# Performance work log

Measured on AMD Instinct MI355X. Metric: run time of the kernel, lower is better.

## Reference

```python
import jax, jax.numpy as jnp
import numpy as np

N1, N2, C = 1024, 1024, 128
H = 2 * C  # h_dim = in_dim * 2


def setup_inputs() -> dict:
    key = jax.random.key(0)
    ks = jax.random.split(key, 8)
    std = 0.01
    return {
        "X": jax.random.normal(ks[0], (N1, C), dtype=jnp.float32),
        "Y": jax.random.normal(ks[1], (N2, C), dtype=jnp.float32),
        "Wsr": jax.random.normal(ks[2], (C, C), dtype=jnp.float32) * std,
        "Wtg": jax.random.normal(ks[3], (C, C), dtype=jnp.float32) * std,
        "W1": jax.random.normal(ks[4], (H, H), dtype=jnp.float32) * std,
        "b1": jnp.zeros((H,), dtype=jnp.float32),
        "W2": jax.random.normal(ks[5], (1, H), dtype=jnp.float32) * std,
        "b2": jnp.zeros((1,), dtype=jnp.float32),
    }


def reference(X, Y, Wsr, Wtg, W1, b1, W2, b2):
    # project_sr / project_tg (bias-free Linear: x @ W^T)
    Xp = X @ Wsr.T  # [N1, C]
    Yp = Y @ Wtg.T  # [N2, C]
    # First fc_M linear on concat([X_k, Y_k]) == split-weight form:
    # concat(x, y) @ W1^T = x @ W1[:, :C]^T + y @ W1[:, C:]^T
    Xh = Xp @ W1[:, :C].T  # [N1, 2C]
    Yh = Yp @ W1[:, C:].T  # [N2, 2C]
    Hid = jax.nn.relu(Xh[:, None, :] + Yh[None, :, :] + b1)  # [N1, N2, 2C]
    # Second linear 2C -> 1, then squeeze
    M = jnp.einsum('abh,h->ab', Hid, W2[0]) + b2[0]  # [N1, N2]
    return M
```

## Files before the change

### kernel.cpp

```cpp
#include <hip/hip_runtime.h>

#define N1 1024
#define N2 1024
#define CDIM 128
#define HDIM 256


__global__ __launch_bounds__(256) void fold_weights(
    const float* __restrict__ W1, const float* __restrict__ Wsr,
    const float* __restrict__ Wtg, float* __restrict__ Wx,
    float* __restrict__ Wy) {
  int id = blockIdx.x * 256 + threadIdx.x;
  int m  = id / (HDIM * CDIM);
  int r  = id % (HDIM * CDIM);
  int h  = r / CDIM;
  int j  = r % CDIM;
  const float* Wm    = m ? Wtg : Wsr;
  const float* w1row = W1 + (size_t)h * HDIM + (m ? CDIM : 0);
  float acc = 0.f;
#pragma unroll 8
  for (int c = 0; c < CDIM; ++c)
    acc = fmaf(w1row[c], Wm[(size_t)c * CDIM + j], acc);
  (m ? Wy : Wx)[(size_t)h * CDIM + j] = acc;
}

__global__ __launch_bounds__(256) void gemm_ht(
    const float* __restrict__ X, const float* __restrict__ Y,
    const float* __restrict__ Wx, const float* __restrict__ Wy,
    const float* __restrict__ b1, float* __restrict__ XhT,
    float* __restrict__ YhT) {
  const float* A = blockIdx.z ? Y : X;
  const float* W = blockIdx.z ? Wy : Wx;
  float*       O = blockIdx.z ? YhT : XhT;
  const bool useBias = (blockIdx.z == 0);

  __shared__ float Al[64][132];
  __shared__ float Wl[128][68];

  const int t  = threadIdx.x;
  const int n0 = blockIdx.x * 64;
  const int h0 = blockIdx.y * 64;

#pragma unroll
  for (int it = 0; it < 8; ++it) {
    int row = it * 8 + (t >> 5);
    int col = (t & 31) * 4;
    *(float4*)(&Al[row][col]) =
        *(const float4*)(&A[(size_t)(n0 + row) * CDIM + col]);
  }
#pragma unroll
  for (int it = 0; it < 8; ++it) {
    int h = it * 8 + (t >> 5);
    int k = (t & 31) * 4;
    float4 w = *(const float4*)(&W[(size_t)(h0 + h) * CDIM + k]);
    Wl[k + 0][h] = w.x;
    Wl[k + 1][h] = w.y;
    Wl[k + 2][h] = w.z;
    Wl[k + 3][h] = w.w;
  }
  __syncthreads();

  const int tx = t & 15;
  const int ty = t >> 4;
  float acc[4][4];
#pragma unroll
  for (int i = 0; i < 4; ++i)
#pragma unroll
    for (int j = 0; j < 4; ++j) acc[i][j] = 0.f;

  for (int k4 = 0; k4 < CDIM; k4 += 4) {
    float a_[4][4];
#pragma unroll
    for (int i = 0; i < 4; ++i) {
      float4 v = *(const float4*)(&Al[ty * 4 + i][k4]);
      a_[i][0] = v.x; a_[i][1] = v.y; a_[i][2] = v.z; a_[i][3] = v.w;
    }
#pragma unroll
    for (int kk = 0; kk < 4; ++kk) {
      float4 w = *(const float4*)(&Wl[k4 + kk][tx * 4]);
      float wj[4] = {w.x, w.y, w.z, w.w};
#pragma unroll
      for (int i = 0; i < 4; ++i)
#pragma unroll
        for (int j = 0; j < 4; ++j)
          acc[i][j] = fmaf(a_[i][kk], wj[j], acc[i][j]);
    }
  }

#pragma unroll
  for (int j = 0; j < 4; ++j) {
    int h = h0 + tx * 4 + j;
    float b = useBias ? b1[h] : 0.f;
    float4 v = {acc[0][j] + b, acc[1][j] + b, acc[2][j] + b, acc[3][j] + b};
    *(float4*)(&O[(size_t)h * N1 + n0 + ty * 4]) = v;
  }
}

__global__ __launch_bounds__(256, 4) void pairwise_half(
    const float* __restrict__ XhT, const float* __restrict__ YhT,
    const float* __restrict__ W2, float* __restrict__ Pbase) {
  __shared__ float Xl[64][64];
  __shared__ float Yl[64][64];

  const int t  = threadIdx.x;
  const int b0 = blockIdx.x * 64;
  const int a0 = blockIdx.y * 64;
  const int hb = blockIdx.z * 64;
  float* P = Pbase + (size_t)blockIdx.z * ((size_t)N1 * N2);

#pragma unroll
  for (int it = 0; it < 4; ++it) {
    int idx = it * 256 + t;
    int hl  = idx >> 4;
    int c4  = (idx & 15) * 4;
    *(float4*)(&Xl[hl][c4]) =
        *(const float4*)(&XhT[(size_t)(hb + hl) * N1 + a0 + c4]);
    *(float4*)(&Yl[hl][c4]) =
        *(const float4*)(&YhT[(size_t)(hb + hl) * N2 + b0 + c4]);
  }
  __syncthreads();

  const int tx = t & 15;
  const int ty = t >> 4;

  float acc[4][4];
#pragma unroll
  for (int i = 0; i < 4; ++i)
#pragma unroll
    for (int j = 0; j < 4; ++j) acc[i][j] = 0.f;

#pragma unroll 2
  for (int h4 = 0; h4 < 64; h4 += 4) {
    float4 w4 = *(const float4*)(&W2[hb + h4]);
    float wh[4] = {w4.x, w4.y, w4.z, w4.w};
#pragma unroll
    for (int hh = 0; hh < 4; ++hh) {
      float4 xv = *(const float4*)(&Xl[h4 + hh][ty * 4]);
      float4 yv = *(const float4*)(&Yl[h4 + hh][tx * 4]);
      float xa[4] = {xv.x, xv.y, xv.z, xv.w};
      float yb[4] = {yv.x, yv.y, yv.z, yv.w};
#pragma unroll
      for (int i = 0; i < 4; ++i)
#pragma unroll
        for (int j = 0; j < 4; ++j) {
          float s = xa[i] + yb[j];
          acc[i][j] = fmaf(fmaxf(s, 0.f), wh[hh], acc[i][j]);
        }
    }
  }

#pragma unroll
  for (int i = 0; i < 4; ++i) {
    int a = a0 + ty * 4 + i;
    float4 v = {acc[i][0], acc[i][1], acc[i][2], acc[i][3]};
    *(float4*)(&P[(size_t)a * N2 + b0 + tx * 4]) = v;
  }
}

__global__ __launch_bounds__(256) void finalize(
    const float* __restrict__ P0, const float* __restrict__ P1,
    const float* __restrict__ P2, const float* __restrict__ P3,
    const float* __restrict__ b2, float* __restrict__ out) {
  int i4 = blockIdx.x * 256 + threadIdx.x;
  float4 a = ((const float4*)P0)[i4];
  float4 b = ((const float4*)P1)[i4];
  float4 c = ((const float4*)P2)[i4];
  float4 d = ((const float4*)P3)[i4];
  const float bb = b2[0];
  float4 o = {a.x + b.x + c.x + d.x + bb, a.y + b.y + c.y + d.y + bb,
              a.z + b.z + c.z + d.z + bb, a.w + b.w + c.w + d.w + bb};
  ((float4*)out)[i4] = o;
}

extern "C" void kernel_launch(void* const* d_in, const int* in_sizes, int n_in,
                              void* d_out, int out_size, void* d_ws,
                              size_t ws_size, hipStream_t stream) {
  const float* X   = (const float*)d_in[0];
  const float* Y   = (const float*)d_in[1];
  const float* Wsr = (const float*)d_in[2];
  const float* Wtg = (const float*)d_in[3];
  const float* W1  = (const float*)d_in[4];
  const float* b1  = (const float*)d_in[5];
  const float* W2  = (const float*)d_in[6];
  const float* b2  = (const float*)d_in[7];
  float* out = (float*)d_out;

  float* ws  = (float*)d_ws;
  float* Wx  = ws;
  float* Wy  = ws + 32768;
  float* XhT = ws + 65536;
  float* YhT = ws + 65536 + 262144;
  float* P   = ws + 589824;

  fold_weights<<<256, 256, 0, stream>>>(W1, Wsr, Wtg, Wx, Wy);
  gemm_ht<<<dim3(16, 4, 2), 256, 0, stream>>>(X, Y, Wx, Wy, b1, XhT, YhT);
  pairwise_half<<<dim3(16, 16, 4), 256, 0, stream>>>(XhT, YhT, W2, P);
  finalize<<<1024, 256, 0, stream>>>(P, P + 1048576, P + 2097152,
                                     P + 3145728, b2, out);
}
```

Baseline: 112.2 us.

## Widen pairwise tile to 64x128 with 4x8 per-thread outputs and swizzled Y layout

The pairwise kernel now covers 128 columns of b per block instead of 64, and each thread computes a 4x8 output patch. This halves the grid along b and raises the number of outputs per shared-memory load. Y is stored in LDS with an interleaved column swizzle so each thread's two float4 reads and its contiguous 8-wide output strip line up. Launch bounds drop to 2 blocks per SM to leave room for the larger accumulator array, which lowers occupancy and halves the block count to 512.

```diff
diff --git a/kernel.cpp b/kernel.cpp
--- a/kernel.cpp
+++ b/kernel.cpp
@@ -96,14 +96,14 @@
   }
 }
 
-__global__ __launch_bounds__(256, 4) void pairwise_half(
+__global__ __launch_bounds__(256, 2) void pairwise_part(
     const float* __restrict__ XhT, const float* __restrict__ YhT,
     const float* __restrict__ W2, float* __restrict__ Pbase) {
   __shared__ float Xl[64][64];
-  __shared__ float Yl[64][64];
+  __shared__ float Yl[64][128];
 
   const int t  = threadIdx.x;
-  const int b0 = blockIdx.x * 64;
+  const int b0 = blockIdx.x * 128;
   const int a0 = blockIdx.y * 64;
   const int hb = blockIdx.z * 64;
   float* P = Pbase + (size_t)blockIdx.z * ((size_t)N1 * N2);
@@ -115,45 +115,62 @@
     int c4  = (idx & 15) * 4;
     *(float4*)(&Xl[hl][c4]) =
         *(const float4*)(&XhT[(size_t)(hb + hl) * N1 + a0 + c4]);
-    *(float4*)(&Yl[hl][c4]) =
-        *(const float4*)(&YhT[(size_t)(hb + hl) * N2 + b0 + c4]);
+  }
+#pragma unroll
+  for (int it = 0; it < 8; ++it) {
+    int idx = it * 256 + t;
+    int hl  = idx >> 5;
+    int c   = idx & 31;
+    int pos = (c >> 1) | ((c & 1) << 4);
+    *(float4*)(&Yl[hl][pos * 4]) =
+        *(const float4*)(&YhT[(size_t)(hb + hl) * N2 + b0 + c * 4]);
   }
   __syncthreads();
 
   const int tx = t & 15;
   const int ty = t >> 4;
 
-  float acc[4][4];
+  float acc[4][8];
 #pragma unroll
   for (int i = 0; i < 4; ++i)
 #pragma unroll
-    for (int j = 0; j < 4; ++j) acc[i][j] = 0.f;
-
-#pragma unroll 2
+    for (int j = 0; j < 8; ++j) acc[i][j] = 0.f;
+
   for (int h4 = 0; h4 < 64; h4 += 4) {
-    float4 w4 = *(const float4*)(&W2[hb + h4]);
-    float wh[4] = {w4.x, w4.y, w4.z, w4.w};
+    const float4 w4 = *(const float4*)(&W2[hb + h4]);
+    const float wh[4] = {w4.x, w4.y, w4.z, w4.w};
 #pragma unroll
     for (int hh = 0; hh < 4; ++hh) {
-      float4 xv = *(const float4*)(&Xl[h4 + hh][ty * 4]);
-      float4 yv = *(const float4*)(&Yl[h4 + hh][tx * 4]);
-      float xa[4] = {xv.x, xv.y, xv.z, xv.w};
-      float yb[4] = {yv.x, yv.y, yv.z, yv.w};
-#pragma unroll
-      for (int i = 0; i < 4; ++i)
-#pragma unroll
-        for (int j = 0; j < 4; ++j) {
-          float s = xa[i] + yb[j];
-          acc[i][j] = fmaf(fmaxf(s, 0.f), wh[hh], acc[i][j]);
+      const int h = h4 + hh;
+      float4 xv = *(const float4*)(&Xl[h][ty * 4]);
+      float4 yv0 = *(const float4*)(&Yl[h][tx * 4]);
+      float4 yv1 = *(const float4*)(&Yl[h][64 + tx * 4]);
+      const float xa[4] = {xv.x, xv.y, xv.z, xv.w};
+      const float yb[8] = {yv0.x, yv0.y, yv0.z, yv0.w,
+                           yv1.x, yv1.y, yv1.z, yv1.w};
+      const float w = wh[hh];
+#pragma unroll
+      for (int i = 0; i < 4; ++i) {
+#pragma unroll
+        for (int j = 0; j < 8; j += 2) {
+          float s0 = xa[i] + yb[j];
+          float s1 = xa[i] + yb[j + 1];
+          float r0 = fmaxf(s0, 0.f);
+          float r1 = fmaxf(s1, 0.f);
+          acc[i][j]     = fmaf(r0, w, acc[i][j]);
+          acc[i][j + 1] = fmaf(r1, w, acc[i][j + 1]);
         }
+      }
     }
   }
 
 #pragma unroll
   for (int i = 0; i < 4; ++i) {
     int a = a0 + ty * 4 + i;
-    float4 v = {acc[i][0], acc[i][1], acc[i][2], acc[i][3]};
-    *(float4*)(&P[(size_t)a * N2 + b0 + tx * 4]) = v;
+    float4 v0 = {acc[i][0], acc[i][1], acc[i][2], acc[i][3]};
+    float4 v1 = {acc[i][4], acc[i][5], acc[i][6], acc[i][7]};
+    *(float4*)(&P[(size_t)a * N2 + b0 + tx * 8])     = v0;
+    *(float4*)(&P[(size_t)a * N2 + b0 + tx * 8 + 4]) = v1;
   }
 }
 
@@ -194,7 +211,7 @@
 
   fold_weights<<<256, 256, 0, stream>>>(W1, Wsr, Wtg, Wx, Wy);
   gemm_ht<<<dim3(16, 4, 2), 256, 0, stream>>>(X, Y, Wx, Wy, b1, XhT, YhT);
-  pairwise_half<<<dim3(16, 16, 4), 256, 0, stream>>>(XhT, YhT, W2, P);
+  pairwise_part<<<dim3(8, 16, 4), 256, 0, stream>>>(XhT, YhT, W2, P);
   finalize<<<1024, 256, 0, stream>>>(P, P + 1048576, P + 2097152,
                                      P + 3145728, b2, out);
 }
```

New measurement: 114.9 us. 1.02x slower.
